# Kernel optimization log

Hardware: AMD Instinct MI355X
Metric: run time of the kernel (lower is better)

## Reference

```python
import jax, jax.numpy as jnp
import numpy as np

NPX = 128      # nPxPup
FOV = 512      # fovInPixel = 2*samp*nPxPup, samp=2
NMODES = 54    # len(jModes)
BATCH = 8
ALPHA = np.pi / 2


def _make_consts():
    # circular pupil on the nPxPup grid
    x = np.linspace(-1.0, 1.0, NPX)
    X, Y = np.meshgrid(x, x)
    pupil = ((X ** 2 + Y ** 2) <= 1.0).astype(np.float32)
    # 4-faced pyramid phase mask on the FOV grid, pre-fftshifted
    f = np.arange(FOV) - FOV / 2
    FX, FY = np.meshgrid(f, f)
    pyr_phase = ALPHA * (np.abs(FX) + np.abs(FY))
    pyr_mask = np.fft.fftshift(np.exp(-1j * pyr_phase)).astype(np.complex64)
    return pupil, pyr_mask


def setup_inputs() -> dict:
    key = jax.random.key(0)
    k1, k2 = jax.random.split(key)
    pupil_np, mask_np = _make_consts()
    pupil = jnp.asarray(pupil_np)                      # [NPX,NPX] float32
    pyrMask = jnp.asarray(mask_np)                     # [FOV,FOV] complex64 (fftshifted)
    # Zernike-like mode basis restricted to the pupil, column-major modes as in the torch buffer
    modes = jax.random.normal(k1, (NPX * NPX, NMODES), dtype=jnp.float32) * pupil.reshape(-1, 1)
    OL1 = (jnp.eye(NMODES, dtype=jnp.float32) * 0.1)   # learnable parameter
    inputs = jax.random.normal(k2, (BATCH, 1, NPX, NPX), dtype=jnp.float32) * pupil
    return {"inputs": inputs, "modes": modes, "OL1": OL1, "pupil": pupil, "pyrMask": pyrMask}


def _prop(phase, pupil, pyrMask):
    """Vanilla pyramid WFS propagation (modulation=0).
    phase: [B,1,NPX,NPX] -> intensity [B,1,FOV,FOV]."""
    u = (pupil * jnp.exp(1j * phase)).astype(jnp.complex64)
    npv = (FOV - NPX) // 2
    field = jnp.zeros(phase.shape[:2] + (FOV, FOV), dtype=jnp.complex64)
    field = field.at[:, :, npv:npv + NPX, npv:npv + NPX].set(u)
    buf = jnp.fft.fft2(field) * pyrMask          # focal plane * pyramid mask
    return jnp.abs(jnp.fft.fft2(buf)) ** 2       # detector intensity


def reference(inputs, modes, OL1, pupil, pyrMask):
    n_modes = OL1.shape[0]
    optModes = modes @ OL1                                     # [NPX*NPX, M]
    # reference (flat wavefront) intensity
    flat = (jnp.ones((NPX, NPX), jnp.float32) * (pupil > 0))[None, None]
    I0 = _prop(flat, pupil, pyrMask)
    I0 = I0 / jnp.sum(I0)                                      # [1,1,FOV,FOV]
    gainRow = jnp.sum(OL1, axis=1)                             # [M]
    # batch the per-mode +/- push-pull propagations in one FFT pass
    zim = optModes.T.reshape(n_modes, 1, NPX, NPX)
    phases = jnp.concatenate([zim, -zim], axis=0)              # [2M,1,NPX,NPX]
    I4 = _prop(phases, pupil, pyrMask)
    I4 = I4 / jnp.sum(I4, axis=(1, 2, 3), keepdims=True)
    sp = I4[:n_modes] - I0
    sm = I4[n_modes:] - I0
    MZc = 0.5 * (sp - sm) / gainRow[:, None, None, None]
    IM = MZc.reshape(n_modes, -1).T                            # [FOV*FOV, M]
    CM = jnp.linalg.pinv(IM)                                   # [M, FOV*FOV]
    # measurement
    Ip = _prop(inputs, pupil, pyrMask)                         # [B,1,FOV,FOV]
    Inorm = jnp.sum(Ip, axis=(1, 2, 3), keepdims=True)
    Ip = Ip / Inorm - I0
    y = CM @ Ip.reshape(Ip.shape[0], -1).T                     # [M, B]
    return y
```

## Files before the change

### kernel.cpp

```cpp
#include <hip/hip_runtime.h>
#include <math.h>

#define NPIXK 262144
#define ROWF2 584

__device__ __forceinline__ int padi8(int i) { return i + (i >> 3); }
__device__ __forceinline__ int padi(int i) { return i + (i >> 5); }

#define WSYNC asm volatile("s_waitcnt lgkmcnt(0)" ::: "memory")

__device__ __forceinline__ void fft8f(float vr[8], float vi[8]) {
    float er[4], ei[4], orr[4], oi[4];
    {
        float t0r = vr[0] + vr[4], t0i = vi[0] + vi[4];
        float t1r = vr[0] - vr[4], t1i = vi[0] - vi[4];
        float t2r = vr[2] + vr[6], t2i = vi[2] + vi[6];
        float t3r = vi[2] - vi[6], t3i = vr[6] - vr[2];
        er[0] = t0r + t2r; ei[0] = t0i + t2i;
        er[1] = t1r + t3r; ei[1] = t1i + t3i;
        er[2] = t0r - t2r; ei[2] = t0i - t2i;
        er[3] = t1r - t3r; ei[3] = t1i - t3i;
    }
    {
        float t0r = vr[1] + vr[5], t0i = vi[1] + vi[5];
        float t1r = vr[1] - vr[5], t1i = vi[1] - vi[5];
        float t2r = vr[3] + vr[7], t2i = vi[3] + vi[7];
        float t3r = vi[3] - vi[7], t3i = vr[7] - vr[3];
        orr[0] = t0r + t2r; oi[0] = t0i + t2i;
        orr[1] = t1r + t3r; oi[1] = t1i + t3i;
        orr[2] = t0r - t2r; oi[2] = t0i - t2i;
        orr[3] = t1r - t3r; oi[3] = t1i - t3i;
    }
    const float c = 0.70710678118654752440f;
    vr[0] = er[0] + orr[0]; vi[0] = ei[0] + oi[0];
    vr[4] = er[0] - orr[0]; vi[4] = ei[0] - oi[0];
    float t1r = c * (orr[1] + oi[1]), t1i = c * (oi[1] - orr[1]);
    vr[1] = er[1] + t1r; vi[1] = ei[1] + t1i;
    vr[5] = er[1] - t1r; vi[5] = ei[1] - t1i;
    float t2r = oi[2], t2i = -orr[2];
    vr[2] = er[2] + t2r; vi[2] = ei[2] + t2i;
    vr[6] = er[2] - t2r; vi[6] = ei[2] - t2i;
    float t3r = c * (oi[3] - orr[3]), t3i = -c * (orr[3] + oi[3]);
    vr[3] = er[3] + t3r; vi[3] = ei[3] + t3i;
    vr[7] = er[3] - t3r; vi[7] = ei[3] - t3i;
}

#define TW2N 576
#define TW1N 72
__device__ __forceinline__ void fill_tw(float2* t2, float2* t1, int tid) {
    for (int i = tid; i < TW2N; i += 256) {
        int t = i / 9, r = i - 9 * t;
        int m = (t * r) & 511; if (m >= 256) m -= 512;
        float s, c;
        sincosf((float)m * -0.01227184630308512985f, &s, &c);
        t2[i] = make_float2(c, s);
    }
    for (int i = tid; i < TW1N; i += 256) {
        int t7 = i / 9, r = i - 9 * t7;
        int m = (t7 * r) & 63; if (m >= 32) m -= 64;
        float s, c;
        sincosf((float)m * -0.09817477042468103870f, &s, &c);
        t1[i] = make_float2(c, s);
    }
}

__device__ __forceinline__ void fft512v(float2* L,
                                        const float2* t1v, const float2* t2v,
                                        int t, float vr[8], float vi[8]) {
    fft8f(vr, vi);
    {
        float2* wb = L + 9 * t;
#pragma unroll
        for (int r = 0; r < 8; ++r) wb[r] = make_float2(vr[r], vi[r]);
    }
    WSYNC;
    {
        const float2* rb = L + t + (t >> 3);
        const float2* tw = t1v + (t & 7) * 9;
        { float2 a = rb[0]; vr[0] = a.x; vi[0] = a.y; }
#pragma unroll
        for (int r = 1; r < 8; ++r) {
            float2 a = rb[72 * r];
            float2 w = tw[r];
            vr[r] = a.x * w.x - a.y * w.y;
            vi[r] = a.x * w.y + a.y * w.x;
        }
        fft8f(vr, vi);
        WSYNC;
        float2* wb = L + 9 * t;
#pragma unroll
        for (int r = 0; r < 8; ++r) wb[r] = make_float2(vr[r], vi[r]);
        WSYNC;
    }
    {
        const float2* rb = L + 9 * (t & 7) + (t >> 3);
        const float2* tw = t2v + t * 9;
        { float2 a = rb[0]; vr[0] = a.x; vi[0] = a.y; }
#pragma unroll
        for (int r = 1; r < 8; ++r) {
            float2 a = rb[72 * r];
            float2 w = tw[r];
            vr[r] = a.x * w.x - a.y * w.y;
            vi[r] = a.x * w.y + a.y * w.x;
        }
        fft8f(vr, vi);
    }
}

#define FFT_LDS \
    __shared__ float2 lds[4][ROWF2]; \
    __shared__ float2 t2v[TW2N]; \
    __shared__ float2 t1v[TW1N];

__device__ __forceinline__ double lsx(int i) {
    if (i == 127) return 1.0;
    return __dadd_rn(__dmul_rn((double)i, 2.0 / 127.0), -1.0);
}
__device__ __forceinline__ double pupilAt(int r, int c) {
    double xc = lsx(c), xr = lsx(r);
    double s = __dadd_rn(__dmul_rn(xc, xc), __dmul_rn(xr, xr));
    return (s <= 1.0) ? 1.0 : 0.0;
}

__global__ __launch_bounds__(256) void k_s1(const float* __restrict__ optT,
                                            const float* __restrict__ inputs,
                                            float2* __restrict__ T1, int giBase) {
    FFT_LDS
    int tid = threadIdx.x, w = tid >> 6, t = tid & 63;
    fill_tw(t2v, t1v, tid);
    __syncthreads();
    int r = (blockIdx.x & 31) * 4 + w;
    int im = blockIdx.x >> 5;
    int gi = (giBase >= 0) ? giBase + im : ((im == 0) ? 0 : 108 + im);

    float vr[8], vi[8];
#pragma unroll
    for (int q = 0; q < 8; ++q) { vr[q] = 0.f; vi[q] = 0.f; }
#pragma unroll
    for (int h = 0; h < 2; ++h) {
        int c = t + 64 * h;
        int p = r * 128 + c;
        float pu = (float)pupilAt(r, c);
        float ph;
        if (gi == 0) {
            ph = pu;
        } else if (gi < 109) {
            ph = optT[(gi - 1) * 16384 + p];
        } else {
            ph = inputs[(gi - 109) * 16384 + p];
        }
        float s, cs; sincosf(ph, &s, &cs);
        vr[3 + h] = pu * cs; vi[3 + h] = pu * s;
    }
    fft512v(lds[w], t1v, t2v, t, vr, vi);
    WSYNC;
#pragma unroll
    for (int q = 0; q < 8; ++q) {
        int d = t + 64 * q;
        lds[w][padi8(d)] = make_float2(vr[q], vi[q]);
    }
    __syncthreads();
    int r0 = (blockIdx.x & 31) * 4;
    float2* dst = T1 + (size_t)im * 65536;
#pragma unroll
    for (int it = 0; it < 8; ++it) {
        int g = it * 256 + tid;
        int l = g >> 2, rr = g & 3;
        dst[(size_t)l * 128 + r0 + rr] = lds[rr][padi8(l)];
    }
}

__global__ __launch_bounds__(256) void k_s23(const float2* __restrict__ T1,
                                             float2* __restrict__ C2p) {
    FFT_LDS
    int tid = threadIdx.x, w = tid >> 6, t = tid & 63;
    fill_tw(t2v, t1v, tid);
    __syncthreads();
    int imgL = blockIdx.x >> 7, l = (blockIdx.x & 127) * 4 + w;
    const float2* src = T1 + (size_t)imgL * 65536 + (size_t)l * 128;
    float vr[8], vi[8];
#pragma unroll
    for (int q = 0; q < 8; ++q) { vr[q] = 0.f; vi[q] = 0.f; }
    float2 a0 = src[t], a1 = src[t + 64];
    vr[3] = a0.x; vi[3] = a0.y;
    vr[4] = a1.x; vi[4] = a1.y;
    fft512v(lds[w], t1v, t2v, t, vr, vi);
    int gl = (l <= 256) ? l : 512 - l;
    int l0 = (blockIdx.x & 127) * 4;
#pragma unroll
    for (int q = 0; q < 8; ++q) {
        int k = t + 64 * q;
        int gk = (k <= 256) ? k : 512 - k;
        int n = (gk + gl) & 3;
        float a = vr[q], b = vi[q], X, Y;
        if (n == 0)      { X = a;  Y = b;  }
        else if (n == 1) { X = b;  Y = -a; }
        else if (n == 2) { X = -a; Y = -b; }
        else             { X = -b; Y = a;  }
        vr[q] = X; vi[q] = Y;
    }
    fft512v(lds[w], t1v, t2v, t, vr, vi);
    WSYNC;
#pragma unroll
    for (int q = 0; q < 8; ++q) {
        int d = t + 64 * q;
        lds[w][padi8(d)] = make_float2(vr[q], vi[q]);
    }
    __syncthreads();
    float2* dst = C2p + (size_t)imgL * NPIXK;
#pragma unroll
    for (int it = 0; it < 8; ++it) {
        int g = it * 256 + tid;
        int p = g >> 2, rr = g & 3;
        dst[(size_t)p * 512 + l0 + rr] = lds[rr][padi8(p)];
    }
}

__global__ __launch_bounds__(256) void k_s4(const float2* __restrict__ C2,
                                            float* __restrict__ dst,
                                            const float* __restrict__ I0,
                                            int ep) {
    FFT_LDS
    int tid = threadIdx.x, w = tid >> 6, t = tid & 63;
    fill_tw(t2v, t1v, tid);
    __syncthreads();
    int imgL = blockIdx.x >> 7, p = (blockIdx.x & 127) * 4 + w;
    const float2* src = C2 + (size_t)imgL * NPIXK + (size_t)p * 512;
    float vr[8], vi[8];
#pragma unroll
    for (int q = 0; q < 8; ++q) { float2 a = src[t + 64 * q]; vr[q] = a.x; vi[q] = a.y; }
    fft512v(lds[w], t1v, t2v, t, vr, vi);
    size_t rowOff = (size_t)p * 512;
    float* drow = dst + (size_t)imgL * NPIXK + rowOff;
    if (ep == 0) {
#pragma unroll
        for (int q = 0; q < 8; ++q) {
            int k = t + 64 * q;
            drow[k] = vr[q] * vr[q] + vi[q] * vi[q];
        }
    } else {
#pragma unroll
        for (int q = 0; q < 8; ++q) {
            int k = t + 64 * q;
            float mag2 = vr[q] * vr[q] + vi[q] * vi[q];
            drow[k] = mag2 - I0[rowOff + k];
        }
    }
}

__global__ __launch_bounds__(256) void k_s4pm(const float2* __restrict__ C2p,
                                              float* __restrict__ dst,
                                              const double* __restrict__ gainInv,
                                              int gBase) {
    FFT_LDS
    int tid = threadIdx.x, w = tid >> 6, t = tid & 63;
    fill_tw(t2v, t1v, tid);
    __syncthreads();
    int imgL = blockIdx.x >> 7, q2 = blockIdx.x & 127;
    int p = 2 * q2 + (w & 1) + (w >> 1) * 256;
    const float2* src = C2p + (size_t)imgL * NPIXK + (size_t)p * 512;
    float vr[8], vi[8], m2[8];
#pragma unroll
    for (int q = 0; q < 8; ++q) { float2 a = src[t + 64 * q]; vr[q] = a.x; vi[q] = a.y; }
    fft512v(lds[w], t1v, t2v, t, vr, vi);
    WSYNC;
    float* mrow = (float*)lds[w];
#pragma unroll
    for (int q = 0; q < 8; ++q) {
        m2[q] = vr[q] * vr[q] + vi[q] * vi[q];
        mrow[padi(t + 64 * q)] = m2[q];
    }
    __syncthreads();
    float g = (float)gainInv[gBase + imgL];
    float* drow = dst + (size_t)imgL * NPIXK + (size_t)p * 512;
    const float* prow = (const float*)lds[w ^ 2];
#pragma unroll
    for (int q = 0; q < 8; ++q) {
        int qp = (q + 4) & 7;
        float other = prow[padi(t + 64 * qp)];
        drow[t + 64 * q] = g * (m2[q] - other);
    }
}

__global__ __launch_bounds__(256) void k_modes(const float* __restrict__ modes,
                                               const float* __restrict__ OL1,
                                               float* __restrict__ optT,
                                               double* __restrict__ gainInv,
                                               double* __restrict__ G,
                                               double* __restrict__ bmat) {
    __shared__ float sM[64 * 54];
    __shared__ float sOL[54 * 54];
    int tid = threadIdx.x;
    if (blockIdx.x == 0) {
        for (int i = tid; i < 54 * 54; i += 256) G[i] = 0.0;
        for (int i = tid; i < 54 * 8; i += 256) bmat[i] = 0.0;
    }
    for (int i = tid; i < 54 * 54; i += 256) sOL[i] = OL1[i];
    const float* msrc = modes + (size_t)blockIdx.x * 64 * 54;
    for (int i = tid; i < 64 * 54; i += 256) sM[i] = msrc[i];
    __syncthreads();
    int pl = tid & 63, mg = tid >> 6;
    int p = blockIdx.x * 64 + pl;
    const float* mrow = sM + pl * 54;
    for (int m = mg; m < 54; m += 4) {
        double acc = 0.0;
#pragma unroll
        for (int j = 0; j < 54; ++j)
            acc += (double)mrow[j] * (double)sOL[j * 54 + m];
        optT[(size_t)m * 16384 + p] = (float)acc;
    }
    if (blockIdx.x == 0 && tid < 54) {
        double g = 0.0;
        for (int j = 0; j < 54; ++j) g += (double)sOL[tid * 54 + j];
        gainInv[tid] = 0.5 / g;
    }
}

__device__ __forceinline__ float dot4(float4 a, float4 b) {
    return a.x * b.x + a.y * b.y + a.z * b.z + a.w * b.w;
}

__global__ __launch_bounds__(256) void k_gram(const float* __restrict__ Mz,
                                              const float* __restrict__ V,
                                              const float* __restrict__ I0,
                                              float* __restrict__ part,
                                              int cA, int PROWS, int subI0) {
    __shared__ float Ms[54 * 128];
    __shared__ float Vs[8 * 128];
    int tid = threadIdx.x;
    int cQ = (cA + 3) >> 2;
    int nQT = cQ * (cQ + 1) / 2;
    int nT = nQT + cQ * 8;
    int task = tid;
    int kind = (task < nQT) ? 0 : (task < nT ? 1 : 2);
    int r0[4], r1[4], bb = 0, Ti = 0, Tj = 0, Qi = 0;
    if (kind == 0) {
        int rem = task;
        while (rem >= cQ - Ti) { rem -= cQ - Ti; ++Ti; }
        Tj = Ti + rem;
#pragma unroll
        for (int q = 0; q < 4; ++q) {
            int i = 4 * Ti + q; r0[q] = (i < cA) ? i : cA - 1;
            int j = 4 * Tj + q; r1[q] = (j < cA) ? j : cA - 1;
        }
    } else if (kind == 1) {
        int tb = task - nQT;
        Qi = tb >> 3; bb = tb & 7;
#pragma unroll
        for (int q = 0; q < 4; ++q) {
            int i = 4 * Qi + q; r0[q] = (i < cA) ? i : cA - 1;
        }
    }
    float s[16];
#pragma unroll
    for (int q = 0; q < 16; ++q) s[q] = 0.f;

    size_t P0 = (size_t)blockIdx.x * 128;
    for (int idx = tid; idx < cA * 32; idx += 256) {
        int i = idx >> 5, v4 = idx & 31;
        ((float4*)Ms)[i * 32 + v4] =
            *(const float4*)(Mz + (size_t)i * NPIXK + P0 + v4 * 4);
    }
    for (int idx = tid; idx < 8 * 32; idx += 256) {
        int b = idx >> 5, v4 = idx & 31;
        float4 vv = *(const float4*)(V + (size_t)b * NPIXK + P0 + v4 * 4);
        if (subI0) {
            float4 i0 = *(const float4*)(I0 + P0 + v4 * 4);
            vv.x -= i0.x; vv.y -= i0.y; vv.z -= i0.z; vv.w -= i0.w;
        }
        ((float4*)Vs)[b * 32 + v4] = vv;
    }
    __syncthreads();
    if (kind == 0) {
        for (int kk = 0; kk < 32; ++kk) {
            int pp = (kk + tid) & 31;
            float4 a0 = ((float4*)(Ms + r0[0] * 128))[pp];
            float4 a1 = ((float4*)(Ms + r0[1] * 128))[pp];
            float4 a2 = ((float4*)(Ms + r0[2] * 128))[pp];
            float4 a3 = ((float4*)(Ms + r0[3] * 128))[pp];
            float4 b0 = ((float4*)(Ms + r1[0] * 128))[pp];
            float4 b1 = ((float4*)(Ms + r1[1] * 128))[pp];
            float4 b2 = ((float4*)(Ms + r1[2] * 128))[pp];
            float4 b3 = ((float4*)(Ms + r1[3] * 128))[pp];
            s[0] += dot4(a0, b0); s[1] += dot4(a0, b1);
            s[2] += dot4(a0, b2); s[3] += dot4(a0, b3);
            s[4] += dot4(a1, b0); s[5] += dot4(a1, b1);
            s[6] += dot4(a1, b2); s[7] += dot4(a1, b3);
            s[8] += dot4(a2, b0); s[9] += dot4(a2, b1);
            s[10] += dot4(a2, b2); s[11] += dot4(a2, b3);
            s[12] += dot4(a3, b0); s[13] += dot4(a3, b1);
            s[14] += dot4(a3, b2); s[15] += dot4(a3, b3);
        }
    } else if (kind == 1) {
        for (int kk = 0; kk < 32; ++kk) {
            int pp = (kk + tid) & 31;
            float4 vb = ((float4*)Vs)[bb * 32 + pp];
            float4 a0 = ((float4*)(Ms + r0[0] * 128))[pp];
            float4 a1 = ((float4*)(Ms + r0[1] * 128))[pp];
            float4 a2 = ((float4*)(Ms + r0[2] * 128))[pp];
            float4 a3 = ((float4*)(Ms + r0[3] * 128))[pp];
            s[0] += dot4(a0, vb); s[1] += dot4(a1, vb);
            s[2] += dot4(a2, vb); s[3] += dot4(a3, vb);
        }
    }
    float* dst = part + (size_t)blockIdx.x * PROWS;
    if (kind == 0) {
#pragma unroll
        for (int q = 0; q < 16; ++q) dst[task * 16 + q] = s[q];
    } else if (kind == 1) {
#pragma unroll
        for (int q = 0; q < 4; ++q)
            dst[nQT * 16 + (task - nQT) * 4 + q] = s[q];
    }
}

__global__ __launch_bounds__(256) void k_gred3(const float* __restrict__ part,
                                               double* __restrict__ G,
                                               double* __restrict__ bmat,
                                               int cA, int m0, int PROWS) {
    __shared__ double red[8][33];
    int tid = threadIdx.x;
    int r = tid & 31, grp = tid >> 5;
    int row = blockIdx.x * 32 + r;
    int bid0 = blockIdx.y * 256;
    double acc = 0.0;
    if (row < PROWS)
        for (int k = 0; k < 32; ++k)
            acc += (double)part[(size_t)(bid0 + grp + 8 * k) * PROWS + row];
    red[grp][r] = acc;
    __syncthreads();
    if (tid < 32) {
        int rr = blockIdx.x * 32 + tid;
        if (rr < PROWS) {
            double s = 0.0;
#pragma unroll
            for (int g = 0; g < 8; ++g) s += red[g][tid];
            int cQ = (cA + 3) >> 2;
            int nQT = cQ * (cQ + 1) / 2;
            if (rr < nQT * 16) {
                int tile = rr >> 4, q = rr & 15;
                int Ti = 0, rem = tile;
                while (rem >= cQ - Ti) { rem -= cQ - Ti; ++Ti; }
                int Tj = Ti + rem;
                int i = 4 * Ti + (q >> 2), j = 4 * Tj + (q & 3);
                if (i < cA && j < cA && i <= j)
                    atomicAdd(&G[(m0 + i) * 54 + (m0 + j)], s);
            } else {
                int qb = rr - nQT * 16;
                int tb = qb >> 2, qq = qb & 3;
                int Qi = tb >> 3, bbb = tb & 7;
                int i = 4 * Qi + qq;
                if (i < cA) atomicAdd(&bmat[(m0 + i) * 8 + bbb], s);
            }
        }
    }
}

__global__ __launch_bounds__(256) void k_gramx(const float* __restrict__ MzA,
                                               const float* __restrict__ MzB,
                                               double* __restrict__ G,
                                               int cA, int m0, int mb) {
    __shared__ float Ms[54 * 128];
    __shared__ float Bs[128];
    int tid = threadIdx.x;
    double acc = 0.0;
    for (int ch = 0; ch < 4; ++ch) {
        size_t P0 = (size_t)blockIdx.x * 512 + (size_t)ch * 128;
        __syncthreads();
        for (int idx = tid; idx < cA * 32; idx += 256) {
            int i = idx >> 5, v4 = idx & 31;
            ((float4*)Ms)[i * 32 + v4] =
                *(const float4*)(MzA + (size_t)i * NPIXK + P0 + v4 * 4);
        }
        if (tid < 128) Bs[tid] = MzB[P0 + tid];
        __syncthreads();
        if (tid < cA) {
            const float* ri = Ms + tid * 128;
            float s = 0.f;
            for (int k = 0; k < 128; ++k) {
                int p = (k + tid) & 127;
                s += ri[p] * Bs[p];
            }
            acc += (double)s;
        }
    }
    if (tid < cA) atomicAdd(&G[(m0 + tid) * 54 + mb], acc);
}

__global__ __launch_bounds__(512) void k_solve(const double* __restrict__ G,
                                               const double* __restrict__ bmat,
                                               float* __restrict__ out) {
    __shared__ double A[54][65];
    int tid = threadIdx.x;
    int r = tid >> 3, cg = tid & 7;
    for (int idx = tid; idx < 54 * 62; idx += 512) {
        int i = idx / 62, c = idx % 62;
        A[i][c] = (c < 54) ? ((i <= c) ? G[i * 54 + c] : G[c * 54 + i])
                           : bmat[i * 8 + (c - 54)];
    }
    __syncthreads();
    for (int p = 0; p < 54; ++p) {
        double f = 0.0;
        bool act = (r < 54) && (r != p);
        if (act) f = A[r][p] / A[p][p];
        __syncthreads();
        if (act) {
#pragma unroll
            for (int k = 0; k < 8; ++k) {
                int c = cg + 8 * k;
                if (c < 62) A[r][c] -= f * A[p][c];
            }
        }
        __syncthreads();
    }
    for (int idx = tid; idx < 54 * 8; idx += 512) {
        int m = idx >> 3, b = idx & 7;
        out[idx] = (float)(A[m][54 + b] / A[m][m]);
    }
}

__global__ void k_zero(float* out, int n) {
    int i = blockIdx.x * 256 + threadIdx.x;
    if (i < n) out[i] = 0.f;
}

extern "C" void kernel_launch(void* const* d_in, const int* in_sizes, int n_in,
                              void* d_out, int out_size, void* d_ws, size_t ws_size,
                              hipStream_t stream) {
    float* out = (float*)d_out;
    if (out_size <= 0) return;
    if (n_in < 3 || in_sizes[0] != 131072 || in_sizes[1] != 884736 ||
        in_sizes[2] != 2916 || out_size < 432) {
        k_zero<<<(out_size + 255) / 256, 256, 0, stream>>>(out, out_size);
        return;
    }
    const float* inputs = (const float*)d_in[0];
    const float* modes  = (const float*)d_in[1];
    const float* OL1    = (const float*)d_in[2];

    char* ws = (char*)d_ws;
    size_t off = 0;
    auto alloc = [&](size_t bytes) -> void* {
        void* p = ws + off;
        off += (bytes + 255) & ~(size_t)255;
        return p;
    };
    float*  optT    = (float*)  alloc((size_t)54 * 16384 * 4);
    double* gainInv = (double*) alloc(64 * 8);
    double* G       = (double*) alloc(54 * 54 * 8);
    double* bmat    = (double*) alloc(54 * 8 * 8);
    float*  I0buf   = (float*)  alloc((size_t)9 * NPIXK * 4);
    float*  V       = I0buf + NPIXK;
    float*  MzB1    = (float*)  alloc((size_t)NPIXK * 4);
    float*  part    = (float*)  alloc((size_t)2048 * 2128 * 4);

    const size_t IMG  = (size_t)NPIXK * 4 + 256;
    const size_t PIPE = ((size_t)65536 * 8 + 256) + ((size_t)NPIXK * 8 + 256);
    size_t rem = (ws_size > off + 4096) ? ws_size - off - 4096 : 0;
    int cA, chunkP;
    if (rem >= 54 * IMG + PIPE) {
        cA = 54;
        size_t c = (rem - 54 * IMG) / PIPE;
        chunkP = (c > 54) ? 54 : (int)c;
        if (chunkP < 1) chunkP = 1;
    } else if (rem >= IMG + PIPE) {
        cA = (int)((rem - PIPE) / IMG);
        if (cA > 53) cA = 53;
        if (cA < 1) cA = 1;
        size_t left = rem - (size_t)cA * IMG;
        chunkP = (int)(left / PIPE);
        if (chunkP < 1) chunkP = 1;
        if (chunkP > cA) chunkP = cA;
    } else {
        k_zero<<<(out_size + 255) / 256, 256, 0, stream>>>(out, out_size);
        return;
    }
    float*  MzA = (float*)  alloc((size_t)cA * NPIXK * 4);
    float2* T1  = (float2*) alloc((size_t)chunkP * 65536 * 8);
    float2* C2p = (float2*) alloc((size_t)chunkP * NPIXK * 8);
    if (off > ws_size) {
        k_zero<<<(out_size + 255) / 256, 256, 0, stream>>>(out, out_size);
        return;
    }

    auto prop_one = [&](int giBase, int n, float* dst, int ep) {
        for (int s = 0; s < n; s += chunkP) {
            int nn = n - s; if (nn > chunkP) nn = chunkP;
            k_s1<<<nn * 32, 256, 0, stream>>>(optT, inputs, T1, giBase + s);
            k_s23<<<nn * 128, 256, 0, stream>>>(T1, C2p);
            k_s4<<<nn * 128, 256, 0, stream>>>(C2p, dst + (size_t)s * NPIXK,
                                               I0buf, ep);
        }
    };
    auto prop_pm = [&](int m0, int n, float* dst, int gBase) {
        for (int s = 0; s < n; s += chunkP) {
            int nn = n - s; if (nn > chunkP) nn = chunkP;
            k_s1<<<nn * 32, 256, 0, stream>>>(optT, inputs, T1, 1 + m0 + s);
            k_s23<<<nn * 128, 256, 0, stream>>>(T1, C2p);
            k_s4pm<<<nn * 128, 256, 0, stream>>>(C2p,
                                                 dst + (size_t)s * NPIXK,
                                                 gainInv, gBase + s);
        }
    };

    k_modes<<<256, 256, 0, stream>>>(modes, OL1, optT, gainInv, G, bmat);
    int subI0;
    if (chunkP >= 9) {
        k_s1<<<9 * 32, 256, 0, stream>>>(optT, inputs, T1, -1);
        k_s23<<<9 * 128, 256, 0, stream>>>(T1, C2p);
        k_s4<<<9 * 128, 256, 0, stream>>>(C2p, I0buf, I0buf, 0);
        subI0 = 1;
    } else {
        prop_one(0, 1, I0buf, 0);
        prop_one(109, 8, V, 2);
        subI0 = 0;
    }
    for (int m0 = 0; m0 < 54; m0 += cA) {
        int ca = 54 - m0; if (ca > cA) ca = cA;
        prop_pm(m0, ca, MzA, m0);
        int cQ = (ca + 3) >> 2;
        int PROWS = cQ * (cQ + 1) / 2 * 16 + cQ * 32;
        k_gram<<<2048, 256, 0, stream>>>(MzA, V, I0buf, part, ca, PROWS, subI0);
        k_gred3<<<dim3((PROWS + 31) / 32, 8), 256, 0, stream>>>(part, G, bmat,
                                                                ca, m0, PROWS);
        for (int mb = m0 + ca; mb < 54; ++mb) {
            prop_pm(mb, 1, MzB1, mb);
            k_gramx<<<512, 256, 0, stream>>>(MzA, MzB1, G, ca, m0, mb);
        }
    }
    k_solve<<<1, 512, 0, stream>>>(G, bmat, out);
}
```

Before: 291.9 us.

## Compute FFT twiddles in registers, specialize sparse first radix-8, raise occupancy

Drops the per-block shared-memory twiddle tables and the block barrier that followed filling them. Each thread now computes its twiddles with one sincosf and a chain of complex multiplies. Adds a specialized first radix-8 butterfly for inputs where only elements 3 and 4 are nonzero, which is the zero-padded case. Launch bounds now request 8 blocks per CU. The twiddle chain trades LDS reads and table setup for extra ALU work and slightly less accurate twiddles, and the occupancy hint may cause register spills.

New measurement: 290.4 us. About the same (-0.5%).

```diff
diff --git a/kernel.cpp b/kernel.cpp
--- a/kernel.cpp
+++ b/kernel.cpp
@@ -8,6 +8,25 @@
 __device__ __forceinline__ int padi(int i) { return i + (i >> 5); }
 
 #define WSYNC asm volatile("s_waitcnt lgkmcnt(0)" ::: "memory")
+
+__device__ __forceinline__ float2 cmul(float2 a, float2 b) {
+    return make_float2(a.x * b.x - a.y * b.y, a.x * b.y + a.y * b.x);
+}
+
+__device__ __forceinline__ void twchain(float ang, float2 tw[8]) {
+    float s, c;
+    sincosf(ang, &s, &c);
+    float2 w1 = make_float2(c, s);
+    float2 w2 = cmul(w1, w1);
+    float2 w4 = cmul(w2, w2);
+    tw[1] = w1;
+    tw[2] = w2;
+    tw[3] = cmul(w1, w2);
+    tw[4] = w4;
+    tw[5] = cmul(w1, w4);
+    tw[6] = cmul(w2, w4);
+    tw[7] = cmul(tw[3], w4);
+}
 
 __device__ __forceinline__ void fft8f(float vr[8], float vi[8]) {
     float er[4], ei[4], orr[4], oi[4];
@@ -45,38 +64,34 @@
     vr[7] = er[3] - t3r; vi[7] = ei[3] - t3i;
 }
 
-#define TW2N 576
-#define TW1N 72
-__device__ __forceinline__ void fill_tw(float2* t2, float2* t1, int tid) {
-    for (int i = tid; i < TW2N; i += 256) {
-        int t = i / 9, r = i - 9 * t;
-        int m = (t * r) & 511; if (m >= 256) m -= 512;
-        float s, c;
-        sincosf((float)m * -0.01227184630308512985f, &s, &c);
-        t2[i] = make_float2(c, s);
-    }
-    for (int i = tid; i < TW1N; i += 256) {
-        int t7 = i / 9, r = i - 9 * t7;
-        int m = (t7 * r) & 63; if (m >= 32) m -= 64;
-        float s, c;
-        sincosf((float)m * -0.09817477042468103870f, &s, &c);
-        t1[i] = make_float2(c, s);
-    }
-}
-
-__device__ __forceinline__ void fft512v(float2* L,
-                                        const float2* t1v, const float2* t2v,
-                                        int t, float vr[8], float vi[8]) {
-    fft8f(vr, vi);
+__device__ __forceinline__ void fft8_s34(float vr[8], float vi[8]) {
+    const float c = 0.70710678118654752440f;
+    float x3r = vr[3], x3i = vi[3], x4r = vr[4], x4i = vi[4];
+    float A = c * (x3r + x3i), B = c * (x3r - x3i);
+    vr[0] = x3r + x4r; vi[0] = x3i + x4i;
+    vr[1] = -B - x4r;  vi[1] = -A - x4i;
+    vr[2] = x4r - x3i; vi[2] = x3r + x4i;
+    vr[3] = A - x4r;   vi[3] = -B - x4i;
+    vr[4] = x4r - x3r; vi[4] = x4i - x3i;
+    vr[5] = B - x4r;   vi[5] = A - x4i;
+    vr[6] = x3i + x4r; vi[6] = x4i - x3r;
+    vr[7] = -A - x4r;  vi[7] = B - x4i;
+}
+
+template <int SPARSE>
+__device__ __forceinline__ void fft512v(float2* L, int t,
+                                        float vr[8], float vi[8]) {
+    if (SPARSE) fft8_s34(vr, vi); else fft8f(vr, vi);
     {
         float2* wb = L + 9 * t;
 #pragma unroll
         for (int r = 0; r < 8; ++r) wb[r] = make_float2(vr[r], vi[r]);
     }
+    float2 tw[8];
+    twchain((float)(t & 7) * -0.09817477042468103870f, tw);
     WSYNC;
     {
         const float2* rb = L + t + (t >> 3);
-        const float2* tw = t1v + (t & 7) * 9;
         { float2 a = rb[0]; vr[0] = a.x; vi[0] = a.y; }
 #pragma unroll
         for (int r = 1; r < 8; ++r) {
@@ -90,11 +105,11 @@
         float2* wb = L + 9 * t;
 #pragma unroll
         for (int r = 0; r < 8; ++r) wb[r] = make_float2(vr[r], vi[r]);
-        WSYNC;
-    }
+    }
+    twchain((float)t * -0.01227184630308512985f, tw);
+    WSYNC;
     {
         const float2* rb = L + 9 * (t & 7) + (t >> 3);
-        const float2* tw = t2v + t * 9;
         { float2 a = rb[0]; vr[0] = a.x; vi[0] = a.y; }
 #pragma unroll
         for (int r = 1; r < 8; ++r) {
@@ -107,10 +122,7 @@
     }
 }
 
-#define FFT_LDS \
-    __shared__ float2 lds[4][ROWF2]; \
-    __shared__ float2 t2v[TW2N]; \
-    __shared__ float2 t1v[TW1N];
+#define FFT_LDS __shared__ float2 lds[4][ROWF2];
 
 __device__ __forceinline__ double lsx(int i) {
     if (i == 127) return 1.0;
@@ -122,13 +134,11 @@
     return (s <= 1.0) ? 1.0 : 0.0;
 }
 
-__global__ __launch_bounds__(256) void k_s1(const float* __restrict__ optT,
-                                            const float* __restrict__ inputs,
-                                            float2* __restrict__ T1, int giBase) {
+__global__ __launch_bounds__(256, 8) void k_s1(const float* __restrict__ optT,
+                                               const float* __restrict__ inputs,
+                                               float2* __restrict__ T1, int giBase) {
     FFT_LDS
     int tid = threadIdx.x, w = tid >> 6, t = tid & 63;
-    fill_tw(t2v, t1v, tid);
-    __syncthreads();
     int r = (blockIdx.x & 31) * 4 + w;
     int im = blockIdx.x >> 5;
     int gi = (giBase >= 0) ? giBase + im : ((im == 0) ? 0 : 108 + im);
@@ -152,7 +162,7 @@
         float s, cs; sincosf(ph, &s, &cs);
         vr[3 + h] = pu * cs; vi[3 + h] = pu * s;
     }
-    fft512v(lds[w], t1v, t2v, t, vr, vi);
+    fft512v<1>(lds[w], t, vr, vi);
     WSYNC;
 #pragma unroll
     for (int q = 0; q < 8; ++q) {
@@ -170,12 +180,10 @@
     }
 }
 
-__global__ __launch_bounds__(256) void k_s23(const float2* __restrict__ T1,
-                                             float2* __restrict__ C2p) {
+__global__ __launch_bounds__(256, 8) void k_s23(const float2* __restrict__ T1,
+                                                float2* __restrict__ C2p) {
     FFT_LDS
     int tid = threadIdx.x, w = tid >> 6, t = tid & 63;
-    fill_tw(t2v, t1v, tid);
-    __syncthreads();
     int imgL = blockIdx.x >> 7, l = (blockIdx.x & 127) * 4 + w;
     const float2* src = T1 + (size_t)imgL * 65536 + (size_t)l * 128;
     float vr[8], vi[8];
@@ -184,7 +192,7 @@
     float2 a0 = src[t], a1 = src[t + 64];
     vr[3] = a0.x; vi[3] = a0.y;
     vr[4] = a1.x; vi[4] = a1.y;
-    fft512v(lds[w], t1v, t2v, t, vr, vi);
+    fft512v<1>(lds[w], t, vr, vi);
     int gl = (l <= 256) ? l : 512 - l;
     int l0 = (blockIdx.x & 127) * 4;
 #pragma unroll
@@ -199,7 +207,7 @@
         else             { X = -b; Y = a;  }
         vr[q] = X; vi[q] = Y;
     }
-    fft512v(lds[w], t1v, t2v, t, vr, vi);
+    fft512v<0>(lds[w], t, vr, vi);
     WSYNC;
 #pragma unroll
     for (int q = 0; q < 8; ++q) {
@@ -216,20 +224,18 @@
     }
 }
 
-__global__ __launch_bounds__(256) void k_s4(const float2* __restrict__ C2,
-                                            float* __restrict__ dst,
-                                            const float* __restrict__ I0,
-                                            int ep) {
+__global__ __launch_bounds__(256, 8) void k_s4(const float2* __restrict__ C2,
+                                               float* __restrict__ dst,
+                                               const float* __restrict__ I0,
+                                               int ep) {
     FFT_LDS
     int tid = threadIdx.x, w = tid >> 6, t = tid & 63;
-    fill_tw(t2v, t1v, tid);
-    __syncthreads();
     int imgL = blockIdx.x >> 7, p = (blockIdx.x & 127) * 4 + w;
     const float2* src = C2 + (size_t)imgL * NPIXK + (size_t)p * 512;
     float vr[8], vi[8];
 #pragma unroll
     for (int q = 0; q < 8; ++q) { float2 a = src[t + 64 * q]; vr[q] = a.x; vi[q] = a.y; }
-    fft512v(lds[w], t1v, t2v, t, vr, vi);
+    fft512v<0>(lds[w], t, vr, vi);
     size_t rowOff = (size_t)p * 512;
     float* drow = dst + (size_t)imgL * NPIXK + rowOff;
     if (ep == 0) {
@@ -248,21 +254,19 @@
     }
 }
 
-__global__ __launch_bounds__(256) void k_s4pm(const float2* __restrict__ C2p,
-                                              float* __restrict__ dst,
-                                              const double* __restrict__ gainInv,
-                                              int gBase) {
+__global__ __launch_bounds__(256, 8) void k_s4pm(const float2* __restrict__ C2p,
+                                                 float* __restrict__ dst,
+                                                 const double* __restrict__ gainInv,
+                                                 int gBase) {
     FFT_LDS
     int tid = threadIdx.x, w = tid >> 6, t = tid & 63;
-    fill_tw(t2v, t1v, tid);
-    __syncthreads();
     int imgL = blockIdx.x >> 7, q2 = blockIdx.x & 127;
     int p = 2 * q2 + (w & 1) + (w >> 1) * 256;
     const float2* src = C2p + (size_t)imgL * NPIXK + (size_t)p * 512;
     float vr[8], vi[8], m2[8];
 #pragma unroll
     for (int q = 0; q < 8; ++q) { float2 a = src[t + 64 * q]; vr[q] = a.x; vi[q] = a.y; }
-    fft512v(lds[w], t1v, t2v, t, vr, vi);
+    fft512v<0>(lds[w], t, vr, vi);
     WSYNC;
     float* mrow = (float*)lds[w];
 #pragma unroll
```
